# Optimization experiments

Hardware: AMD Instinct MI355X
Metric: run time of the kernel (lower is better)

## Reference

```python
import jax, jax.numpy as jnp
import numpy as np

H = 8          # multihead_num (also groups of the Conv1d)
LN_EPS = 1e-5  # torch.nn.LayerNorm default


def _gconv(x, w):
    """Grouped Conv1d, kernel=3, stride=1, 'same' reflect padding, no bias.
    x: [B, C_in, L], w: [C_out, C_in//H, K] (torch OIH layout)."""
    xp = jnp.pad(x, ((0, 0), (0, 0), (1, 1)), mode='reflect')
    return jax.lax.conv_general_dilated(
        xp, w, window_strides=(1,), padding='VALID',
        feature_group_count=H, dimension_numbers=('NCH', 'OIH', 'NCH'))


def setup_inputs() -> dict:
    key = jax.random.key(0)
    ks = jax.random.split(key, 5)
    B, C, L = 8, 512, 1024
    q = jax.random.normal(ks[0], (B, C, L), jnp.float32)
    k = jax.random.normal(ks[1], (B, C, L), jnp.float32)
    # causal mask: 1 above the diagonal -> -1e9 subtracted pre-softmax
    mask = jnp.triu(jnp.ones((L, L), jnp.float32), k=1)
    # init_params: std = sqrt(2 / (C_out + C_in/groups))
    std = float(np.sqrt(2.0 / (C + C // H)))
    wq = jax.random.normal(ks[2], (C, C // H, 3), jnp.float32) * std
    wk = jax.random.normal(ks[3], (C, C // H, 3), jnp.float32) * std
    wv = jax.random.normal(ks[4], (C, C // H, 3), jnp.float32) * std
    gamma = jnp.ones((C,), jnp.float32)
    beta = jnp.zeros((C,), jnp.float32)
    return {"q": q, "k": k, "mask": mask, "wq": wq, "wk": wk, "wv": wv,
            "gamma": gamma, "beta": beta}


def reference(q, k, mask, wq, wk, wv, gamma, beta):
    init = q                               # residual branch, [B, C, L]
    B, C, L = q.shape
    D = C // H                             # head dim
    v = k                                  # inputs list of length 2 -> v = k

    qh = _gconv(q, wq).reshape(B, H, D, L)  # split(dim=1)+cat(dim=0) == head axis
    kh = _gconv(k, wk).reshape(B, H, D, L)
    vh = _gconv(v, wv).reshape(B, H, D, L)

    # scores: q^T k per head; NOTE: scaled by sqrt(multihead_num), as in source
    scores = jnp.einsum('bhdl,bhdm->bhlm', qh, kh) / jnp.sqrt(
        jnp.asarray(H, qh.dtype))
    scores = scores - 1e9 * mask           # mask broadcast over [B, H]
    att = jax.nn.softmax(scores, axis=-1)  # dropout p=0.0 -> identity

    # o = att @ v^T, then concat heads along channel (head-major order)
    o = jnp.einsum('bhlm,bhdm->blhd', att, vh).reshape(B, L, C)

    # residual add + LayerNorm over channel dim
    x = o + jnp.swapaxes(init, 1, 2)       # [B, L, C]
    mu = jnp.mean(x, axis=-1, keepdims=True)
    var = jnp.mean(jnp.square(x - mu), axis=-1, keepdims=True)
    y = (x - mu) * jax.lax.rsqrt(var + LN_EPS) * gamma + beta
    return jnp.swapaxes(y, 1, 2)           # [B, C, L]
```

## Files before the change

kernel.cpp:

```cpp
#include <hip/hip_runtime.h>
#include <math.h>

#define H 8
#define B 8
#define C 512
#define L 1024
#define D 64
#define LDK 72

typedef __attribute__((ext_vector_type(4))) float f32x4;
typedef __attribute__((ext_vector_type(8))) short bf16x8;

static __device__ __forceinline__ short f2bf(float x) {
    union { float f; unsigned u; } v; v.f = x;
    unsigned r = v.u + 0x7FFFu + ((v.u >> 16) & 1u);
    return (short)(r >> 16);
}
static __device__ __forceinline__ short f2bf_fast(float x) {
    union { float f; unsigned u; } v; v.f = x;
    return (short)((v.u + 0x8000u) >> 16);
}
static __device__ __forceinline__ int pack2(short a, short b) {
    return (int)((unsigned short)a | ((unsigned)(unsigned short)b << 16));
}
static __device__ __forceinline__ float bfs2f(short v) {
    union { unsigned u; float f; } w; w.u = ((unsigned)(unsigned short)v) << 16;
    return w.f;
}
static __device__ __forceinline__ void async16(const void* g, void* s) {
    __builtin_amdgcn_global_load_lds(
        (const __attribute__((address_space(1))) int*)g,
        (__attribute__((address_space(3))) int*)s, 16, 0, 0);
}

__global__ __launch_bounds__(256) void wprep_kernel(
    const float* __restrict__ wq, const float* __restrict__ wk,
    const float* __restrict__ wv, short* __restrict__ wtg)
{
    int idx = blockIdx.x * 256 + threadIdx.x;
    int jj    = idx & 7;
    int quad  = (idx >> 3) & 3;
    int d     = (idx >> 5) & 63;
    int r     = idx >> 11;
    int khalf = r & 1;  r >>= 1;
    int t     = r % 3;  r /= 3;
    int h     = r & 7;
    int conv  = r >> 3;
    const float* w = (conv == 0) ? wq : (conv == 1) ? wk : wv;
    int j_in = khalf * 32 + quad * 8 + jj;
    float v = w[(h * 64 + d) * 192 + j_in * 3 + t];
    if (conv == 0) v *= 0.51012254f;
    wtg[idx] = f2bf(v);
}

__global__ __launch_bounds__(256) void conv_kernel(
    const float* __restrict__ q, const float* __restrict__ k,
    const short* __restrict__ wtg,
    short* __restrict__ qh, short* __restrict__ kh, short* __restrict__ vh)
{
    int bx   = blockIdx.x;
    int tile = bx & 15;
    int h    = (bx >> 4) & 7;
    int b    = (bx >> 7) & 7;
    int src  = bx >> 10;

    __shared__ short xT[66 * LDK];

    int l0  = tile * 64;
    int tid = threadIdx.x;
    int wave = tid >> 6, lane = tid & 63;
    int n = lane & 15, quad = lane >> 4;

    const float* x  = src ? k : q;
    const float* xb = x + (size_t)(b * C + h * 64) * L + l0;

    int c0 = src ? 1 : 0;
    const short* wb0 = wtg + (size_t)((c0 * 8 + h) * 3 * 2) * 2048;
    bf16x8 wf[3][2], wf2[3][2];
    #pragma unroll
    for (int t = 0; t < 3; t++)
        #pragma unroll
        for (int kk = 0; kk < 2; kk++)
            wf[t][kk] = *(const bf16x8*)(wb0 + (t * 2 + kk) * 2048
                                         + (wave * 16 + n) * 32 + quad * 8);
    if (src) {
        const short* wb1 = wtg + (size_t)((2 * 8 + h) * 3 * 2) * 2048;
        #pragma unroll
        for (int t = 0; t < 3; t++)
            #pragma unroll
            for (int kk = 0; kk < 2; kk++)
                wf2[t][kk] = *(const bf16x8*)(wb1 + (t * 2 + kk) * 2048
                                              + (wave * 16 + n) * 32 + quad * 8);
    }

    {
        int j = tid >> 2;
        #pragma unroll
        for (int s = 0; s < 4; s++) {
            int i = (tid & 3) + s * 4;
            float4 v = *(const float4*)(xb + j * L + i * 4);
            int p = 1 + i * 4;
            xT[(p + 0) * LDK + j] = f2bf(v.x);
            xT[(p + 1) * LDK + j] = f2bf(v.y);
            xT[(p + 2) * LDK + j] = f2bf(v.z);
            xT[(p + 3) * LDK + j] = f2bf(v.w);
        }
        if (tid < 64) {
            int gl = (l0 == 0) ? 1 : (l0 - 1);
            xT[0 * LDK + tid] = f2bf(x[(size_t)(b * C + h * 64 + tid) * L + gl]);
        } else if (tid < 128) {
            int j2 = tid - 64;
            int gl = (l0 + 64 >= L) ? (L - 2) : (l0 + 64);
            xT[65 * LDK + j2] = f2bf(x[(size_t)(b * C + h * 64 + j2) * L + gl]);
        }
    }
    __syncthreads();

    f32x4 acc[4], acc2[4];
    #pragma unroll
    for (int bl = 0; bl < 4; bl++) {
        acc[bl]  = (f32x4){0.f, 0.f, 0.f, 0.f};
        acc2[bl] = (f32x4){0.f, 0.f, 0.f, 0.f};
    }

    #pragma unroll
    for (int bl = 0; bl < 4; bl++) {
        #pragma unroll
        for (int t = 0; t < 3; t++) {
            #pragma unroll
            for (int kk = 0; kk < 2; kk++) {
                bf16x8 bf = *(const bf16x8*)&xT[(bl * 16 + n + t) * LDK
                                                + kk * 32 + quad * 8];
                acc[bl] = __builtin_amdgcn_mfma_f32_16x16x32_bf16(
                    wf[t][kk], bf, acc[bl], 0, 0, 0);
                if (src)
                    acc2[bl] = __builtin_amdgcn_mfma_f32_16x16x32_bf16(
                        wf2[t][kk], bf, acc2[bl], 0, 0, 0);
            }
        }
    }

    int bhh = b * H + h;
    short* o1 = src ? kh : qh;
    {
        short* ob = o1 + ((size_t)(bhh * 16 + tile)) * 4096;
        int ch = wave * 2 + (quad >> 1);
        #pragma unroll
        for (int bl = 0; bl < 4; bl++) {
            int l = bl * 16 + n;
            int phys = ch ^ (l & 7);
            int2 v;
            v.x = pack2(f2bf(acc[bl][0]), f2bf(acc[bl][1]));
            v.y = pack2(f2bf(acc[bl][2]), f2bf(acc[bl][3]));
            *(int2*)&ob[l * 64 + phys * 8 + (quad & 1) * 4] = v;
        }
    }
    if (src) {
        short* vb = vh + ((size_t)(bhh * 16 + tile)) * 4096;
        #pragma unroll
        for (int bl = 0; bl < 4; bl++)
            #pragma unroll
            for (int r = 0; r < 4; r++) {
                int d = wave * 16 + quad * 4 + r;
                int l = bl * 16 + n;
                int phys = (bl * 2 + (n >> 3)) ^ (d & 7);
                vb[d * 64 + phys * 8 + (l & 7)] = f2bf(acc2[bl][r]);
            }
    }
}

__global__ __launch_bounds__(256, 4) void flash_kernel(
    const short* __restrict__ qh, const short* __restrict__ kh,
    const short* __restrict__ vh, short* __restrict__ ot)
{
    __shared__ __align__(16) short lds[20480];

    int bx = blockIdx.x;
    int bh = bx & 63;
    int qt = 15 - (bx >> 6);
    int h  = bh & 7, b = bh >> 3;

    int tid  = threadIdx.x;
    int wave = tid >> 6, lane = tid & 63;
    int n    = lane & 15, quad = lane >> 4;

    const short* Qg    = qh + ((size_t)(bh * 16 + qt)) * 4096;
    const short* Kbase = kh + (size_t)bh * 65536;
    const short* Vbase = vh + (size_t)bh * 65536;

    {
        int ci = wave * 64 + lane;
        async16((const int4*)Qg + ci,           lds + wave * 512);
        async16((const int4*)Qg + ci + 256,     lds + 2048 + wave * 512);
        async16((const int4*)Kbase + ci,        lds + 4096 + wave * 512);
        async16((const int4*)Kbase + ci + 256,  lds + 4096 + 2048 + wave * 512);
        async16((const int4*)Vbase + ci,        lds + 8192 + wave * 512);
        async16((const int4*)Vbase + ci + 256,  lds + 8192 + 2048 + wave * 512);
    }
    __syncthreads();

    int ph0 = quad ^ (n & 7);
    int ph1 = (quad + 4) ^ (n & 7);

    bf16x8 qa0 = *(const bf16x8*)&lds[(wave * 16 + n) * 64 + ph0 * 8];
    bf16x8 qa1 = *(const bf16x8*)&lds[(wave * 16 + n) * 64 + ph1 * 8];

    const bf16x8 ones = {16256,16256,16256,16256,16256,16256,16256,16256};

    f32x4 O0 = {0.f,0.f,0.f,0.f}, O1 = O0, O2 = O0, O3 = O0;
    f32x4 Lacc = {0.f,0.f,0.f,0.f};

    for (int kt = 0; kt <= qt; kt++) {
        if (kt > 0) __syncthreads();
        if (kt < qt) {
            const short* Kg = Kbase + (size_t)(kt + 1) * 4096;
            const short* Vg = Vbase + (size_t)(kt + 1) * 4096;
            int koff = 4096 + (((kt + 1) & 1)) * 8192;
            int ci = wave * 64 + lane;
            async16((const int4*)Kg + ci,       lds + koff + wave * 512);
            async16((const int4*)Kg + ci + 256, lds + koff + 2048 + wave * 512);
            async16((const int4*)Vg + ci,       lds + koff + 4096 + wave * 512);
            async16((const int4*)Vg + ci + 256, lds + koff + 4096 + 2048 + wave * 512);
        }
        const short* Kb = lds + 4096 + (kt & 1) * 8192;
        const short* Vb = Kb + 4096;

        f32x4 s[4];
        #pragma unroll
        for (int bk = 0; bk < 4; bk++) {
            int row = bk * 16 + n;
            bf16x8 kb0 = *(const bf16x8*)&Kb[row * 64 + ph0 * 8];
            bf16x8 kb1 = *(const bf16x8*)&Kb[row * 64 + ph1 * 8];
            f32x4 acc = {0.f,0.f,0.f,0.f};
            acc = __builtin_amdgcn_mfma_f32_16x16x32_bf16(qa0, kb0, acc, 0, 0, 0);
            acc = __builtin_amdgcn_mfma_f32_16x16x32_bf16(qa1, kb1, acc, 0, 0, 0);
            s[bk] = acc;
        }

        if (kt == qt) {
            #pragma unroll
            for (int bk = 0; bk < 4; bk++)
                #pragma unroll
                for (int r = 0; r < 4; r++)
                    if (bk * 16 + n > wave * 16 + quad * 4 + r)
                        s[bk][r] = -INFINITY;
        }

        #pragma unroll
        for (int bk = 0; bk < 4; bk++)
            #pragma unroll
            for (int r = 0; r < 4; r++) {
                int prow = wave * 16 + quad * 4 + r;
                int pch  = (bk * 2 + (n >> 3)) ^ (prow & 7);
                lds[prow * 64 + pch * 8 + (n & 7)] =
                    f2bf_fast(__builtin_amdgcn_exp2f(s[bk][r] - 20.f));
            }

        bf16x8 pa0 = *(const bf16x8*)&lds[(wave * 16 + n) * 64 + ph0 * 8];
        bf16x8 pa1 = *(const bf16x8*)&lds[(wave * 16 + n) * 64 + ph1 * 8];

        Lacc = __builtin_amdgcn_mfma_f32_16x16x32_bf16(pa0, ones, Lacc, 0, 0, 0);
        Lacc = __builtin_amdgcn_mfma_f32_16x16x32_bf16(pa1, ones, Lacc, 0, 0, 0);

        #pragma unroll
        for (int bk = 0; bk < 4; bk++) {
            int row = bk * 16 + n;
            bf16x8 v0 = *(const bf16x8*)&Vb[row * 64 + ph0 * 8];
            bf16x8 v1 = *(const bf16x8*)&Vb[row * 64 + ph1 * 8];
            f32x4* Op = (bk == 0) ? &O0 : (bk == 1) ? &O1 : (bk == 2) ? &O2 : &O3;
            *Op = __builtin_amdgcn_mfma_f32_16x16x32_bf16(pa0, v0, *Op, 0, 0, 0);
            *Op = __builtin_amdgcn_mfma_f32_16x16x32_bf16(pa1, v1, *Op, 0, 0, 0);
        }
    }

    float inv[4];
    #pragma unroll
    for (int r = 0; r < 4; r++) inv[r] = 1.f / Lacc[r];

    __syncthreads();
    short* Eb = lds + 4096;
    #pragma unroll
    for (int bk = 0; bk < 4; bk++) {
        f32x4* Op = (bk == 0) ? &O0 : (bk == 1) ? &O1 : (bk == 2) ? &O2 : &O3;
        #pragma unroll
        for (int r = 0; r < 4; r++)
            Eb[(bk * 16 + n) * LDK + wave * 16 + quad * 4 + r] =
                f2bf_fast((*Op)[r] * inv[r]);
    }
    __syncthreads();
    #pragma unroll
    for (int jj = 0; jj < 2; jj++) {
        int i = tid + jj * 256;
        int d = i >> 3, seg = i & 7;
        int4 v = *(const int4*)&Eb[d * LDK + seg * 8];
        *(int4*)(ot + ((size_t)(b * C) + h * 64 + d) * L + qt * 64 + seg * 8) = v;
    }
}

__global__ __launch_bounds__(512) void ln_kernel(
    const short* __restrict__ ot, const float* __restrict__ q,
    const float* __restrict__ gamma, const float* __restrict__ beta,
    float* __restrict__ y)
{
    int bx = blockIdx.x;
    int tile = bx & 31;
    int b = bx >> 5;
    int l0 = tile * 32;
    int tid = threadIdx.x;
    int li_ = tid & 31, cs = tid >> 5;

    __shared__ float sp[16][33], ssp[16][33];
    __shared__ float mu_s[32], rs_s[32];

    size_t base = ((size_t)b * C + cs * 32) * L + l0 + li_;
    const short* otp = ot + base;
    const float* qp  = q + base;

    float xr[32];
    float s = 0.f, ss = 0.f;
    #pragma unroll
    for (int cc = 0; cc < 32; cc++) {
        float x = bfs2f(otp[(size_t)cc * L]) + qp[(size_t)cc * L];
        xr[cc] = x;
        s += x; ss += x * x;
    }
    sp[cs][li_] = s; ssp[cs][li_] = ss;
    __syncthreads();
    if (tid < 32) {
        float t1 = 0.f, t2 = 0.f;
        #pragma unroll
        for (int j = 0; j < 16; j++) { t1 += sp[j][tid]; t2 += ssp[j][tid]; }
        float mean = t1 * (1.f / 512.f);
        float var  = t2 * (1.f / 512.f) - mean * mean;
        mu_s[tid] = mean;
        rs_s[tid] = rsqrtf(var + 1e-5f);
    }
    __syncthreads();
    float mu = mu_s[li_], rs = rs_s[li_];
    float* yp = y + base;
    #pragma unroll
    for (int cc = 0; cc < 32; cc++) {
        int c = cs * 32 + cc;
        yp[(size_t)cc * L] = (xr[cc] - mu) * rs * gamma[c] + beta[c];
    }
}

extern "C" void kernel_launch(void* const* d_in, const int* in_sizes, int n_in,
                              void* d_out, int out_size, void* d_ws, size_t ws_size,
                              hipStream_t stream)
{
    const float* q     = (const float*)d_in[0];
    const float* k     = (const float*)d_in[1];
    const float* wq    = (const float*)d_in[3];
    const float* wk    = (const float*)d_in[4];
    const float* wv    = (const float*)d_in[5];
    const float* gamma = (const float*)d_in[6];
    const float* beta  = (const float*)d_in[7];
    float* y = (float*)d_out;

    const size_t N = (size_t)B * H * L * D;
    short* qh  = (short*)d_ws;
    short* kh  = qh + N;
    short* vh  = kh + N;
    short* ot  = vh + N;
    short* wtg = ot + N;

    wprep_kernel<<<1152, 256, 0, stream>>>(wq, wk, wv, wtg);
    conv_kernel<<<2 * B * H * (L / 64), 256, 0, stream>>>(q, k, wtg, qh, kh, vh);
    flash_kernel<<<B * H * (L / 64), 256, 0, stream>>>(qh, kh, vh, ot);
    ln_kernel<<<B * (L / 32), 512, 0, stream>>>(ot, q, gamma, beta, y);
}
```

Before: 135.6 us.

## Rewrite flash attention with 32x32 MFMA, two waves per block

The flash kernel now uses 128-thread blocks where each wave owns 32 query rows and issues 32x32x16 bf16 MFMAs. It computes S^T through swapped operands and writes P and the output with packed int2 stores instead of scalar shorts. The conv kernel now stages V through shared memory so its global writes are coalesced 16-byte stores, and its input load pattern is reorganised. The goal is fewer MFMA and LDS instructions per tile and better store coalescing, at the cost of fewer waves per block and more registers per thread.

```diff
diff --git a/kernel.cpp b/kernel.cpp
--- a/kernel.cpp
+++ b/kernel.cpp
@@ -9,6 +9,7 @@
 #define LDK 72
 
 typedef __attribute__((ext_vector_type(4))) float f32x4;
+typedef __attribute__((ext_vector_type(16))) float f32x16;
 typedef __attribute__((ext_vector_type(8))) short bf16x8;
 
 static __device__ __forceinline__ short f2bf(float x) {
@@ -64,7 +65,7 @@
     int b    = (bx >> 7) & 7;
     int src  = bx >> 10;
 
-    __shared__ short xT[66 * LDK];
+    __shared__ __align__(16) short xT[66 * LDK];
 
     int l0  = tile * 64;
     int tid = threadIdx.x;
@@ -94,12 +95,12 @@
     }
 
     {
-        int j = tid >> 2;
         #pragma unroll
         for (int s = 0; s < 4; s++) {
-            int i = (tid & 3) + s * 4;
-            float4 v = *(const float4*)(xb + j * L + i * 4);
-            int p = 1 + i * 4;
+            int idx = tid + s * 256;
+            int j = idx >> 4, seg = idx & 15;
+            float4 v = *(const float4*)(xb + j * L + seg * 4);
+            int p = 1 + seg * 4;
             xT[(p + 0) * LDK + j] = f2bf(v.x);
             xT[(p + 1) * LDK + j] = f2bf(v.y);
             xT[(p + 2) * LDK + j] = f2bf(v.z);
@@ -156,7 +157,7 @@
         }
     }
     if (src) {
-        short* vb = vh + ((size_t)(bhh * 16 + tile)) * 4096;
+        __syncthreads();
         #pragma unroll
         for (int bl = 0; bl < 4; bl++)
             #pragma unroll
@@ -164,12 +165,19 @@
                 int d = wave * 16 + quad * 4 + r;
                 int l = bl * 16 + n;
                 int phys = (bl * 2 + (n >> 3)) ^ (d & 7);
-                vb[d * 64 + phys * 8 + (l & 7)] = f2bf(acc2[bl][r]);
+                xT[d * 64 + phys * 8 + (n & 7)] = f2bf(acc2[bl][r]);
             }
-    }
-}
-
-__global__ __launch_bounds__(256, 4) void flash_kernel(
+        __syncthreads();
+        short* vb = vh + ((size_t)(bhh * 16 + tile)) * 4096;
+        #pragma unroll
+        for (int jj = 0; jj < 2; jj++) {
+            int i = tid + jj * 256;
+            *(int4*)(vb + i * 8) = *(const int4*)&xT[i * 8];
+        }
+    }
+}
+
+__global__ __launch_bounds__(128, 2) void flash_kernel(
     const short* __restrict__ qh, const short* __restrict__ kh,
     const short* __restrict__ vh, short* __restrict__ ot)
 {
@@ -181,118 +189,131 @@
     int h  = bh & 7, b = bh >> 3;
 
     int tid  = threadIdx.x;
-    int wave = tid >> 6, lane = tid & 63;
-    int n    = lane & 15, quad = lane >> 4;
+    int wave = tid >> 6;
+    int lane = tid & 63;
+    int m    = lane & 31;
+    int half = lane >> 5;
+    int sw   = m & 7;
 
     const short* Qg    = qh + ((size_t)(bh * 16 + qt)) * 4096;
     const short* Kbase = kh + (size_t)bh * 65536;
     const short* Vbase = vh + (size_t)bh * 65536;
 
-    {
-        int ci = wave * 64 + lane;
-        async16((const int4*)Qg + ci,           lds + wave * 512);
-        async16((const int4*)Qg + ci + 256,     lds + 2048 + wave * 512);
-        async16((const int4*)Kbase + ci,        lds + 4096 + wave * 512);
-        async16((const int4*)Kbase + ci + 256,  lds + 4096 + 2048 + wave * 512);
-        async16((const int4*)Vbase + ci,        lds + 8192 + wave * 512);
-        async16((const int4*)Vbase + ci + 256,  lds + 8192 + 2048 + wave * 512);
-    }
-    __syncthreads();
-
-    int ph0 = quad ^ (n & 7);
-    int ph1 = (quad + 4) ^ (n & 7);
-
-    bf16x8 qa0 = *(const bf16x8*)&lds[(wave * 16 + n) * 64 + ph0 * 8];
-    bf16x8 qa1 = *(const bf16x8*)&lds[(wave * 16 + n) * 64 + ph1 * 8];
+    #pragma unroll
+    for (int s = 0; s < 4; s++) {
+        int ci = s * 128 + tid;
+        int lo = (s * 128 + wave * 64) * 8;
+        async16((const int4*)Qg + ci,    lds + lo);
+        async16((const int4*)Kbase + ci, lds + 4096 + lo);
+        async16((const int4*)Vbase + ci, lds + 8192 + lo);
+    }
+    __syncthreads();
+
+    int row_q = wave * 32 + m;
+
+    bf16x8 qb[4];
+    #pragma unroll
+    for (int st = 0; st < 4; st++)
+        qb[st] = *(const bf16x8*)&lds[row_q * 64 + (((half + 2 * st) ^ sw) * 8)];
 
     const bf16x8 ones = {16256,16256,16256,16256,16256,16256,16256,16256};
 
-    f32x4 O0 = {0.f,0.f,0.f,0.f}, O1 = O0, O2 = O0, O3 = O0;
-    f32x4 Lacc = {0.f,0.f,0.f,0.f};
+    f32x16 O0, O1, Lacc;
+    #pragma unroll
+    for (int r = 0; r < 16; r++) { O0[r] = 0.f; O1[r] = 0.f; Lacc[r] = 0.f; }
 
     for (int kt = 0; kt <= qt; kt++) {
         if (kt > 0) __syncthreads();
         if (kt < qt) {
             const short* Kg = Kbase + (size_t)(kt + 1) * 4096;
             const short* Vg = Vbase + (size_t)(kt + 1) * 4096;
-            int koff = 4096 + (((kt + 1) & 1)) * 8192;
-            int ci = wave * 64 + lane;
-            async16((const int4*)Kg + ci,       lds + koff + wave * 512);
-            async16((const int4*)Kg + ci + 256, lds + koff + 2048 + wave * 512);
-            async16((const int4*)Vg + ci,       lds + koff + 4096 + wave * 512);
-            async16((const int4*)Vg + ci + 256, lds + koff + 4096 + 2048 + wave * 512);
+            int koff = 4096 + ((kt + 1) & 1) * 8192;
+            #pragma unroll
+            for (int s = 0; s < 4; s++) {
+                int ci = s * 128 + tid;
+                int lo = (s * 128 + wave * 64) * 8;
+                async16((const int4*)Kg + ci, lds + koff + lo);
+                async16((const int4*)Vg + ci, lds + koff + 4096 + lo);
+            }
         }
         const short* Kb = lds + 4096 + (kt & 1) * 8192;
         const short* Vb = Kb + 4096;
 
-        f32x4 s[4];
-        #pragma unroll
-        for (int bk = 0; bk < 4; bk++) {
-            int row = bk * 16 + n;
-            bf16x8 kb0 = *(const bf16x8*)&Kb[row * 64 + ph0 * 8];
-            bf16x8 kb1 = *(const bf16x8*)&Kb[row * 64 + ph1 * 8];
-            f32x4 acc = {0.f,0.f,0.f,0.f};
-            acc = __builtin_amdgcn_mfma_f32_16x16x32_bf16(qa0, kb0, acc, 0, 0, 0);
-            acc = __builtin_amdgcn_mfma_f32_16x16x32_bf16(qa1, kb1, acc, 0, 0, 0);
-            s[bk] = acc;
+        f32x16 s0, s1;
+        #pragma unroll
+        for (int r = 0; r < 16; r++) { s0[r] = 0.f; s1[r] = 0.f; }
+        #pragma unroll
+        for (int st = 0; st < 4; st++) {
+            int co = ((half + 2 * st) ^ sw) * 8;
+            bf16x8 ka0 = *(const bf16x8*)&Kb[m * 64 + co];
+            bf16x8 ka1 = *(const bf16x8*)&Kb[(32 + m) * 64 + co];
+            s0 = __builtin_amdgcn_mfma_f32_32x32x16_bf16(ka0, qb[st], s0, 0, 0, 0);
+            s1 = __builtin_amdgcn_mfma_f32_32x32x16_bf16(ka1, qb[st], s1, 0, 0, 0);
         }
 
         if (kt == qt) {
             #pragma unroll
-            for (int bk = 0; bk < 4; bk++)
-                #pragma unroll
-                for (int r = 0; r < 4; r++)
-                    if (bk * 16 + n > wave * 16 + quad * 4 + r)
-                        s[bk][r] = -INFINITY;
-        }
-
-        #pragma unroll
-        for (int bk = 0; bk < 4; bk++)
-            #pragma unroll
-            for (int r = 0; r < 4; r++) {
-                int prow = wave * 16 + quad * 4 + r;
-                int pch  = (bk * 2 + (n >> 3)) ^ (prow & 7);
-                lds[prow * 64 + pch * 8 + (n & 7)] =
-                    f2bf_fast(__builtin_amdgcn_exp2f(s[bk][r] - 20.f));
+            for (int r = 0; r < 16; r++) {
+                int ko = (r & 3) + 8 * (r >> 2) + 4 * half;
+                if (ko > row_q)      s0[r] = -INFINITY;
+                if (32 + ko > row_q) s1[r] = -INFINITY;
             }
-
-        bf16x8 pa0 = *(const bf16x8*)&lds[(wave * 16 + n) * 64 + ph0 * 8];
-        bf16x8 pa1 = *(const bf16x8*)&lds[(wave * 16 + n) * 64 + ph1 * 8];
-
-        Lacc = __builtin_amdgcn_mfma_f32_16x16x32_bf16(pa0, ones, Lacc, 0, 0, 0);
-        Lacc = __builtin_amdgcn_mfma_f32_16x16x32_bf16(pa1, ones, Lacc, 0, 0, 0);
-
-        #pragma unroll
-        for (int bk = 0; bk < 4; bk++) {
-            int row = bk * 16 + n;
-            bf16x8 v0 = *(const bf16x8*)&Vb[row * 64 + ph0 * 8];
-            bf16x8 v1 = *(const bf16x8*)&Vb[row * 64 + ph1 * 8];
-            f32x4* Op = (bk == 0) ? &O0 : (bk == 1) ? &O1 : (bk == 2) ? &O2 : &O3;
-            *Op = __builtin_amdgcn_mfma_f32_16x16x32_bf16(pa0, v0, *Op, 0, 0, 0);
-            *Op = __builtin_amdgcn_mfma_f32_16x16x32_bf16(pa1, v1, *Op, 0, 0, 0);
-        }
-    }
-
-    float inv[4];
-    #pragma unroll
-    for (int r = 0; r < 4; r++) inv[r] = 1.f / Lacc[r];
+        }
+
+        #pragma unroll
+        for (int t = 0; t < 4; t++) {
+            int2 v0, v1;
+            v0.x = pack2(f2bf_fast(__builtin_amdgcn_exp2f(s0[4*t+0] - 20.f)),
+                         f2bf_fast(__builtin_amdgcn_exp2f(s0[4*t+1] - 20.f)));
+            v0.y = pack2(f2bf_fast(__builtin_amdgcn_exp2f(s0[4*t+2] - 20.f)),
+                         f2bf_fast(__builtin_amdgcn_exp2f(s0[4*t+3] - 20.f)));
+            v1.x = pack2(f2bf_fast(__builtin_amdgcn_exp2f(s1[4*t+0] - 20.f)),
+                         f2bf_fast(__builtin_amdgcn_exp2f(s1[4*t+1] - 20.f)));
+            v1.y = pack2(f2bf_fast(__builtin_amdgcn_exp2f(s1[4*t+2] - 20.f)),
+                         f2bf_fast(__builtin_amdgcn_exp2f(s1[4*t+3] - 20.f)));
+            *(int2*)&lds[row_q * 64 + ((t       ^ sw) * 8) + 4 * half] = v0;
+            *(int2*)&lds[row_q * 64 + (((4 + t) ^ sw) * 8) + 4 * half] = v1;
+        }
+
+        bf16x8 pa[4];
+        #pragma unroll
+        for (int st = 0; st < 4; st++)
+            pa[st] = *(const bf16x8*)&lds[row_q * 64 + (((half + 2 * st) ^ sw) * 8)];
+
+        #pragma unroll
+        for (int st = 0; st < 4; st++) {
+            int co = ((half + 2 * st) ^ sw) * 8;
+            bf16x8 vb0 = *(const bf16x8*)&Vb[m * 64 + co];
+            bf16x8 vb1 = *(const bf16x8*)&Vb[(32 + m) * 64 + co];
+            Lacc = __builtin_amdgcn_mfma_f32_32x32x16_bf16(pa[st], ones, Lacc, 0, 0, 0);
+            O0   = __builtin_amdgcn_mfma_f32_32x32x16_bf16(pa[st], vb0,  O0,  0, 0, 0);
+            O1   = __builtin_amdgcn_mfma_f32_32x32x16_bf16(pa[st], vb1,  O1,  0, 0, 0);
+        }
+    }
+
+    float inv[16];
+    #pragma unroll
+    for (int r = 0; r < 16; r++) inv[r] = 1.f / Lacc[r];
 
     __syncthreads();
     short* Eb = lds + 4096;
     #pragma unroll
-    for (int bk = 0; bk < 4; bk++) {
-        f32x4* Op = (bk == 0) ? &O0 : (bk == 1) ? &O1 : (bk == 2) ? &O2 : &O3;
-        #pragma unroll
-        for (int r = 0; r < 4; r++)
-            Eb[(bk * 16 + n) * LDK + wave * 16 + quad * 4 + r] =
-                f2bf_fast((*Op)[r] * inv[r]);
-    }
-    __syncthreads();
-    #pragma unroll
-    for (int jj = 0; jj < 2; jj++) {
-        int i = tid + jj * 256;
+    for (int t = 0; t < 4; t++) {
+        int qoff = 8 * t + 4 * half;
+        int2 v0, v1;
+        v0.x = pack2(f2bf_fast(O0[4*t+0] * inv[4*t+0]), f2bf_fast(O0[4*t+1] * inv[4*t+1]));
+        v0.y = pack2(f2bf_fast(O0[4*t+2] * inv[4*t+2]), f2bf_fast(O0[4*t+3] * inv[4*t+3]));
+        v1.x = pack2(f2bf_fast(O1[4*t+0] * inv[4*t+0]), f2bf_fast(O1[4*t+1] * inv[4*t+1]));
+        v1.y = pack2(f2bf_fast(O1[4*t+2] * inv[4*t+2]), f2bf_fast(O1[4*t+3] * inv[4*t+3]));
+        *(int2*)&Eb[m * 72        + wave * 32 + qoff] = v0;
+        *(int2*)&Eb[(32 + m) * 72 + wave * 32 + qoff] = v1;
+    }
+    __syncthreads();
+    #pragma unroll
+    for (int jj = 0; jj < 4; jj++) {
+        int i = tid + jj * 128;
         int d = i >> 3, seg = i & 7;
-        int4 v = *(const int4*)&Eb[d * LDK + seg * 8];
+        int4 v = *(const int4*)&Eb[d * 72 + seg * 8];
         *(int4*)(ot + ((size_t)(b * C) + h * 64 + d) * L + qt * 64 + seg * 8) = v;
     }
 }
@@ -367,6 +388,6 @@
 
     wprep_kernel<<<1152, 256, 0, stream>>>(wq, wk, wv, wtg);
     conv_kernel<<<2 * B * H * (L / 64), 256, 0, stream>>>(q, k, wtg, qh, kh, vh);
-    flash_kernel<<<B * H * (L / 64), 256, 0, stream>>>(qh, kh, vh, ot);
+    flash_kernel<<<B * H * (L / 64), 128, 0, stream>>>(qh, kh, vh, ot);
     ln_kernel<<<B * (L / 32), 512, 0, stream>>>(ot, q, gamma, beta, y);
 }
```

Result: slower. 140.5 us (+3.6%).
